# Kernel tuning notes

Measured on AMD Instinct MI355X. Metric: run time of the kernel, lower is better.

The kernel has to match this reference:

```python
import jax, jax.numpy as jnp
import numpy as np


def _softmax_kernel(data, proj, is_query, eps=1e-4):
    # data: [b,h,n,d], proj: [m,d] -> features [b,h,n,m]
    d = data.shape[-1]
    data_normalizer = d ** -0.25
    ratio = proj.shape[0] ** -0.5
    data_dash = jnp.einsum('bhnd,md->bhnm', data_normalizer * data, proj)
    diag_data = jnp.sum(data * data, axis=-1, keepdims=True) * 0.5 * (data_normalizer ** 2)
    if is_query:
        stab = jnp.max(data_dash, axis=-1, keepdims=True)
    else:
        stab = jnp.max(data_dash, axis=(-1, -2), keepdims=True)
    stab = jax.lax.stop_gradient(stab)
    return ratio * (jnp.exp(data_dash - diag_data - stab) + eps)


def setup_inputs() -> dict:
    key = jax.random.key(0)
    k1, k2, k3, k4 = jax.random.split(key, 4)
    b, h, n, d, m = 8, 16, 4096, 64, 256
    q = jax.random.normal(k1, (b, h, n, d), dtype=jnp.float32)
    k = jax.random.normal(k2, (b, h, n, d), dtype=jnp.float32)
    v = jax.random.normal(k3, (b, h, n, d), dtype=jnp.float32)
    projection_matrix = jax.random.normal(k4, (m, d), dtype=jnp.float32)
    return {'q': q, 'k': k, 'v': v, 'projection_matrix': projection_matrix}


def reference(q, k, v, projection_matrix):
    # FAVOR+ softmax-kernel features
    q_prime = _softmax_kernel(q, projection_matrix, is_query=True)   # [b,h,n,m]
    k_prime = _softmax_kernel(k, projection_matrix, is_query=False)  # [b,h,n,m]
    # Non-causal linear attention
    k_sum = jnp.sum(k_prime, axis=-2)                                # [b,h,m]
    d_inv = 1.0 / jnp.einsum('bhnm,bhm->bhn', q_prime, k_sum)        # [b,h,n]
    context = jnp.einsum('bhnm,bhne->bhme', k_prime, v)              # [b,h,m,e]
    out = jnp.einsum('bhme,bhnm,bhn->bhne', context, q_prime, d_inv) # [b,h,n,e]
    return out
```

## Files before the change

### kernel.cpp

```cpp
#include <hip/hip_runtime.h>


#define BH 128
#define NN 4096
#define DD 64
#define MM 256
#define NORM 0.35355339059327373f
#define EPS 1e-4f

typedef unsigned short u16;
typedef __attribute__((ext_vector_type(8))) short bfrag;
typedef __attribute__((ext_vector_type(4))) float ffrag;
#define MFMA16(A,B,C) __builtin_amdgcn_mfma_f32_16x16x32_bf16(A,B,C,0,0,0)

__device__ __forceinline__ float u2f(u16 h){ return __uint_as_float(((unsigned)h)<<16); }
__device__ __forceinline__ void splitf(float x, u16 &h, u16 &l){
    unsigned uh = __float_as_uint(x) & 0xffff0000u;
    h = (u16)(uh >> 16);
    float r = x - __uint_as_float(uh);
    l = (u16)(__float_as_uint(r) >> 16);
}

__global__ void p0_proj(const float* __restrict__ proj, u16* __restrict__ phi, u16* __restrict__ plo){
    int idx = blockIdx.x*256 + threadIdx.x;
    u16 h,l; splitf(proj[idx], h, l);
    phi[idx] = h; plo[idx] = l;
}

__global__ __launch_bounds__(256) void p0_vt(const float* __restrict__ vin,
        u16* __restrict__ vthi, u16* __restrict__ vtlo, float* __restrict__ vsum){
    int head = blockIdx.x >> 6;
    int n0 = (blockIdx.x & 63) * 64;
    int t = threadIdx.x;
    __shared__ float tile[64][65];
    {
        int row = t >> 2, c0 = (t & 3) * 16;
        const float* src = vin + ((size_t)head*NN + n0 + row)*64 + c0;
        #pragma unroll
        for (int i=0;i<4;++i){
            float4 x = *(const float4*)(src + i*4);
            tile[row][c0+i*4+0]=x.x; tile[row][c0+i*4+1]=x.y;
            tile[row][c0+i*4+2]=x.z; tile[row][c0+i*4+3]=x.w;
        }
    }
    __syncthreads();
    {
        int e = t >> 2, nq = (t & 3) * 16;
        float s = 0.f;
        unsigned ph[8], pl[8];
        #pragma unroll
        for (int jj=0;jj<8;++jj){
            float x0 = tile[nq+jj*2+0][e];
            float x1 = tile[nq+jj*2+1][e];
            s += x0 + x1;
            u16 h0,l0,h1,l1; splitf(x0,h0,l0); splitf(x1,h1,l1);
            ph[jj] = (unsigned)h0 | ((unsigned)h1<<16);
            pl[jj] = (unsigned)l0 | ((unsigned)l1<<16);
        }
        size_t base = ((size_t)head*64 + e)*NN + n0 + nq;
        uint4 a0; a0.x=ph[0]; a0.y=ph[1]; a0.z=ph[2]; a0.w=ph[3];
        uint4 a1; a1.x=ph[4]; a1.y=ph[5]; a1.z=ph[6]; a1.w=ph[7];
        uint4 b0; b0.x=pl[0]; b0.y=pl[1]; b0.z=pl[2]; b0.w=pl[3];
        uint4 b1; b1.x=pl[4]; b1.y=pl[5]; b1.z=pl[6]; b1.w=pl[7];
        *(uint4*)(vthi + base)     = a0;
        *(uint4*)(vthi + base + 8) = a1;
        *(uint4*)(vtlo + base)     = b0;
        *(uint4*)(vtlo + base + 8) = b1;
        s += __shfl_xor(s, 1);
        s += __shfl_xor(s, 2);
        if ((t & 3) == 0) atomicAdd(vsum + head*64 + e, s);
    }
}

__global__ __launch_bounds__(256) __attribute__((amdgpu_waves_per_eu(2,2)))
void kc_kernel(
        const float* __restrict__ kin, const u16* __restrict__ phi, const u16* __restrict__ plo,
        const u16* __restrict__ vthi, const u16* __restrict__ vtlo,
        float* __restrict__ ctxPart, float* __restrict__ mbArr)
{
    const int blk  = blockIdx.x;
    const int head = blk >> 3;
    const int n0   = (blk & 7) * 512;
    const int t    = threadIdx.x;
    const int w    = t >> 6;
    const int lane = t & 63;
    const int qd   = lane >> 4;
    const int li   = lane & 15;

    __shared__ __attribute__((aligned(16))) u16 knh[32*64], knl[32*64];
    __shared__ __attribute__((aligned(16))) u16 bsh[256*32], bsl[256*32];
    __shared__ float diag_s[32];
    __shared__ float wmax[4];

    bfrag pf[4][2][2];
    #pragma unroll
    for (int mt=0;mt<4;++mt){
        int m = w*64 + mt*16 + li;
        #pragma unroll
        for (int ks=0;ks<2;++ks){
            pf[mt][ks][0] = *(const bfrag*)(phi + m*64 + ks*32 + qd*8);
            pf[mt][ks][1] = *(const bfrag*)(plo + m*64 + ks*32 + qd*8);
        }
    }

    ffrag acc[4][4];
    #pragma unroll
    for (int et=0;et<4;++et)
        #pragma unroll
        for (int mt=0;mt<4;++mt){ ffrag z = {0.f,0.f,0.f,0.f}; acc[et][mt] = z; }
    float ks[4] = {0.f,0.f,0.f,0.f};
    float M = -3.0e38f;

    const float* kg = kin + ((size_t)head*NN + n0)*64;

    for (int sub=0; sub<16; ++sub){
        {
            int row = t >> 3;
            int g   = t & 7;
            const float* src = kg + (size_t)(sub*32 + row)*64 + g*8;
            float4 x0 = *(const float4*)(src);
            float4 x1 = *(const float4*)(src + 4);
            float xs[8] = {x0.x,x0.y,x0.z,x0.w,x1.x,x1.y,x1.z,x1.w};
            bfrag hv, lv;
            float ss = 0.f;
            #pragma unroll
            for (int j=0;j<8;++j){
                float xn = xs[j]*NORM;
                ss += xn*xn;
                u16 hh,ll; splitf(xn,hh,ll);
                hv[j] = (short)hh; lv[j] = (short)ll;
            }
            int gs = g ^ (row & 7);
            *(bfrag*)(knh + row*64 + gs*8) = hv;
            *(bfrag*)(knl + row*64 + gs*8) = lv;
            ss += __shfl_xor(ss, 1);
            ss += __shfl_xor(ss, 2);
            ss += __shfl_xor(ss, 4);
            if ((t & 7) == 0) diag_s[row] = 0.5f*ss;
        }
        __syncthreads();

        ffrag d1[2][4];
        #pragma unroll
        for (int nt=0;nt<2;++nt)
            #pragma unroll
            for (int mt=0;mt<4;++mt){ ffrag z = {0.f,0.f,0.f,0.f}; d1[nt][mt] = z; }
        #pragma unroll
        for (int nt=0;nt<2;++nt){
            int n = nt*16 + li;
            bfrag ah[2], al[2];
            #pragma unroll
            for (int kss=0;kss<2;++kss){
                int gp = (kss*4 + qd) ^ (n & 7);
                ah[kss] = *(const bfrag*)(knh + n*64 + gp*8);
                al[kss] = *(const bfrag*)(knl + n*64 + gp*8);
            }
            #pragma unroll
            for (int mt=0;mt<4;++mt){
                #pragma unroll
                for (int kss=0;kss<2;++kss){
                    d1[nt][mt] = MFMA16(ah[kss], pf[mt][kss][0], d1[nt][mt]);
                    d1[nt][mt] = MFMA16(ah[kss], pf[mt][kss][1], d1[nt][mt]);
                    d1[nt][mt] = MFMA16(al[kss], pf[mt][kss][0], d1[nt][mt]);
                }
            }
        }

        float mx = -3.0e38f;
        #pragma unroll
        for (int nt=0;nt<2;++nt)
            #pragma unroll
            for (int mt=0;mt<4;++mt)
                #pragma unroll
                for (int rg=0;rg<4;++rg) mx = fmaxf(mx, d1[nt][mt][rg]);
        mx = fmaxf(mx, __shfl_xor(mx, 1));
        mx = fmaxf(mx, __shfl_xor(mx, 2));
        mx = fmaxf(mx, __shfl_xor(mx, 4));
        mx = fmaxf(mx, __shfl_xor(mx, 8));
        mx = fmaxf(mx, __shfl_xor(mx, 16));
        mx = fmaxf(mx, __shfl_xor(mx, 32));
        if (lane == 0) wmax[w] = mx;
        __syncthreads();
        float Ms = fmaxf(fmaxf(wmax[0],wmax[1]), fmaxf(wmax[2],wmax[3]));
        float Mn = fmaxf(M, Ms);
        float r  = __expf(M - Mn);
        M = Mn;
        #pragma unroll
        for (int mt=0;mt<4;++mt) ks[mt] *= r;
        #pragma unroll
        for (int et=0;et<4;++et)
            #pragma unroll
            for (int mt=0;mt<4;++mt)
                #pragma unroll
                for (int rg=0;rg<4;++rg) acc[et][mt][rg] *= r;

        float sl[4] = {0.f,0.f,0.f,0.f};
        #pragma unroll
        for (int nt=0;nt<2;++nt){
            float d4[4];
            #pragma unroll
            for (int rg=0;rg<4;++rg) d4[rg] = diag_s[nt*16 + qd*4 + rg];
            #pragma unroll
            for (int mt=0;mt<4;++mt){
                int m = w*64 + mt*16 + li;
                u16 h4[4], l4[4];
                #pragma unroll
                for (int rg=0;rg<4;++rg){
                    float f = __expf(d1[nt][mt][rg] - d4[rg] - M);
                    sl[mt] += f;
                    splitf(f, h4[rg], l4[rg]);
                }
                int g  = nt*2 + (qd>>1);
                int gp = g ^ ((m>>1)&3);
                int off = m*32 + gp*8 + (qd&1)*4;
                *(ushort4*)(bsh + off) = make_ushort4(h4[0],h4[1],h4[2],h4[3]);
                *(ushort4*)(bsl + off) = make_ushort4(l4[0],l4[1],l4[2],l4[3]);
            }
        }
        #pragma unroll
        for (int mt=0;mt<4;++mt){
            float v = sl[mt];
            v += __shfl_xor(v, 16);
            v += __shfl_xor(v, 32);
            ks[mt] += v;
        }
        __syncthreads();

        bfrag bh[4], bl[4];
        #pragma unroll
        for (int mt=0;mt<4;++mt){
            int m = w*64 + mt*16 + li;
            int gp = qd ^ ((m>>1)&3);
            bh[mt] = *(const bfrag*)(bsh + m*32 + gp*8);
            bl[mt] = *(const bfrag*)(bsl + m*32 + gp*8);
        }
        #pragma unroll
        for (int et=0;et<4;++et){
            int e = et*16 + li;
            size_t vb = ((size_t)head*64 + e)*NN + n0 + sub*32 + qd*8;
            bfrag avh = *(const bfrag*)(vthi + vb);
            bfrag avl = *(const bfrag*)(vtlo + vb);
            #pragma unroll
            for (int mt=0;mt<4;++mt){
                acc[et][mt] = MFMA16(avh, bh[mt], acc[et][mt]);
                acc[et][mt] = MFMA16(avh, bl[mt], acc[et][mt]);
                acc[et][mt] = MFMA16(avl, bh[mt], acc[et][mt]);
            }
        }
        __syncthreads();
    }

    float* P = ctxPart + (size_t)blk * (65*256);
    #pragma unroll
    for (int et=0;et<4;++et)
        #pragma unroll
        for (int mt=0;mt<4;++mt)
            #pragma unroll
            for (int rg=0;rg<4;++rg){
                int e = et*16 + qd*4 + rg;
                int m = w*64 + mt*16 + li;
                P[e*256 + m] = acc[et][mt][rg];
            }
    if (qd == 0){
        #pragma unroll
        for (int mt=0;mt<4;++mt) P[64*256 + w*64 + mt*16 + li] = ks[mt];
    }
    if (t == 0) mbArr[blk] = M;
}

__global__ __launch_bounds__(256) void kred(const float* __restrict__ ctxPart,
        const float* __restrict__ mbArr, const float* __restrict__ vsum,
        u16* __restrict__ ctxh, u16* __restrict__ ctxl, float* __restrict__ ksumG){
    int head = blockIdx.x / 65;
    int e = blockIdx.x % 65;
    int m = threadIdx.x;
    float mb[8];
    float mk = -3.0e38f;
    #pragma unroll
    for (int c=0;c<8;++c){ mb[c] = mbArr[head*8+c]; mk = fmaxf(mk, mb[c]); }
    float s = 0.f;
    #pragma unroll
    for (int c=0;c<8;++c){
        float sc = __expf(mb[c] - mk);
        s += sc * ctxPart[((size_t)(head*8+c)*65 + e)*256 + m];
    }
    if (e == 64){
        ksumG[head*256 + m] = s + 4096.0f*EPS;
    } else {
        float val = s + EPS * vsum[head*64 + e];
        u16 h,l; splitf(val,h,l);
        ctxh[((size_t)head*64 + e)*256 + m] = h;
        ctxl[((size_t)head*64 + e)*256 + m] = l;
    }
}

__global__ __launch_bounds__(256) __attribute__((amdgpu_waves_per_eu(2,2)))
void k3_kernel(
        const float* __restrict__ qin, const u16* __restrict__ phi, const u16* __restrict__ plo,
        const u16* __restrict__ ctxh, const u16* __restrict__ ctxl,
        const float* __restrict__ ksumG, float* __restrict__ out)
{
    const int bx   = blockIdx.x;
    const int head = (bx & 7) + 8 * ((bx >> 3) & 15);
    const int n0   = (bx >> 7) * 64;
    const int t    = threadIdx.x;
    const int w    = t >> 6;
    const int lane = t & 63;
    const int qd   = lane >> 4;
    const int li   = lane & 15;

    __shared__ __attribute__((aligned(16))) u16 SM[32768];
    u16* qnh = SM;
    u16* qnl = SM + 4096;
    u16* fh  = SM;
    u16* fl  = SM + 16384;
    __shared__ float diagq[64], drm[64], dinvs[64], wm[4][64];

    {
        int row = t >> 2;
        const float* src = qin + ((size_t)head*NN + n0 + row)*64 + (t&3)*16;
        float ss = 0.f;
        #pragma unroll
        for (int gi=0; gi<2; ++gi){
            int g = (t&3)*2 + gi;
            float4 x0 = *(const float4*)(src + gi*8);
            float4 x1 = *(const float4*)(src + gi*8 + 4);
            float xs[8] = {x0.x,x0.y,x0.z,x0.w,x1.x,x1.y,x1.z,x1.w};
            bfrag hv, lv;
            #pragma unroll
            for (int j=0;j<8;++j){
                float xn = xs[j]*NORM;
                ss += xn*xn;
                u16 hh,ll; splitf(xn,hh,ll);
                hv[j] = (short)hh; lv[j] = (short)ll;
            }
            int gs = g ^ (row & 7);
            *(bfrag*)(qnh + row*64 + gs*8) = hv;
            *(bfrag*)(qnl + row*64 + gs*8) = lv;
        }
        ss += __shfl_xor(ss, 1);
        ss += __shfl_xor(ss, 2);
        if ((t&3) == 0) diagq[row] = 0.5f*ss;
    }

    float4 ks4[4];
    #pragma unroll
    for (int mt=0;mt<4;++mt)
        ks4[mt] = *(const float4*)(ksumG + head*256 + w*64 + mt*16 + qd*4);
    __syncthreads();

    ffrag d1[4][4];
    #pragma unroll
    for (int mt=0;mt<4;++mt)
        #pragma unroll
        for (int nt=0;nt<4;++nt){ ffrag z = {0.f,0.f,0.f,0.f}; d1[mt][nt] = z; }
    #pragma unroll
    for (int kss=0;kss<2;++kss){
        bfrag pfh[4], pfl[4];
        #pragma unroll
        for (int mt=0;mt<4;++mt){
            int m = w*64 + mt*16 + li;
            pfh[mt] = *(const bfrag*)(phi + m*64 + kss*32 + qd*8);
            pfl[mt] = *(const bfrag*)(plo + m*64 + kss*32 + qd*8);
        }
        #pragma unroll
        for (int nt=0;nt<4;++nt){
            int n = nt*16 + li;
            int gp = (kss*4 + qd) ^ (n & 7);
            bfrag bh = *(const bfrag*)(qnh + n*64 + gp*8);
            bfrag bl = *(const bfrag*)(qnl + n*64 + gp*8);
            #pragma unroll
            for (int mt=0;mt<4;++mt){
                d1[mt][nt] = MFMA16(pfh[mt], bh, d1[mt][nt]);
                d1[mt][nt] = MFMA16(pfh[mt], bl, d1[mt][nt]);
                d1[mt][nt] = MFMA16(pfl[mt], bh, d1[mt][nt]);
            }
        }
    }

    #pragma unroll
    for (int nt=0;nt<4;++nt){
        float mx = -3.0e38f;
        #pragma unroll
        for (int mt=0;mt<4;++mt)
            #pragma unroll
            for (int rg=0;rg<4;++rg) mx = fmaxf(mx, d1[mt][nt][rg]);
        mx = fmaxf(mx, __shfl_xor(mx, 16));
        mx = fmaxf(mx, __shfl_xor(mx, 32));
        if (qd == 0) wm[w][nt*16 + li] = mx;
    }
    __syncthreads();
    if (t < 64)
        drm[t] = diagq[t] + fmaxf(fmaxf(wm[0][t], wm[1][t]), fmaxf(wm[2][t], wm[3][t]));
    __syncthreads();

    float ds[4] = {0.f,0.f,0.f,0.f};
    #pragma unroll
    for (int nt=0;nt<4;++nt){
        int n = nt*16 + li;
        float dr = drm[n];
        #pragma unroll
        for (int mt=0;mt<4;++mt){
            float fv[4];
            u16 h4[4], l4[4];
            #pragma unroll
            for (int rg=0;rg<4;++rg){
                fv[rg] = __expf(d1[mt][nt][rg] - dr) + EPS;
                splitf(fv[rg], h4[rg], l4[rg]);
            }
            ds[nt] += fv[0]*ks4[mt].x + fv[1]*ks4[mt].y + fv[2]*ks4[mt].z + fv[3]*ks4[mt].w;
            int G  = w*8 + mt*2 + (qd>>1);
            int Gp = G ^ (li & 7);
            int off = n*256 + Gp*8 + (qd&1)*4;
            *(ushort4*)(fh + off) = make_ushort4(h4[0],h4[1],h4[2],h4[3]);
            *(ushort4*)(fl + off) = make_ushort4(l4[0],l4[1],l4[2],l4[3]);
        }
    }
    #pragma unroll
    for (int nt=0;nt<4;++nt){
        float v = ds[nt];
        v += __shfl_xor(v, 16);
        v += __shfl_xor(v, 32);
        if (qd == 0) wm[w][nt*16 + li] = v;
    }
    __syncthreads();
    if (t < 64)
        dinvs[t] = 1.0f / (wm[0][t] + wm[1][t] + wm[2][t] + wm[3][t]);
    __syncthreads();

    ffrag a2[4];
    #pragma unroll
    for (int nt=0;nt<4;++nt){ ffrag z = {0.f,0.f,0.f,0.f}; a2[nt] = z; }
    const u16* cbh = ctxh + (size_t)head*64*256 + (w*16 + li)*256;
    const u16* cbl = ctxl + (size_t)head*64*256 + (w*16 + li)*256;
    #pragma unroll
    for (int ksm=0; ksm<8; ++ksm){
        bfrag ch = *(const bfrag*)(cbh + ksm*32 + qd*8);
        bfrag cl = *(const bfrag*)(cbl + ksm*32 + qd*8);
        #pragma unroll
        for (int nt=0;nt<4;++nt){
            int n = nt*16 + li;
            int Gp = (ksm*4 + qd) ^ (li & 7);
            bfrag ah2 = *(const bfrag*)(fh + n*256 + Gp*8);
            bfrag al2 = *(const bfrag*)(fl + n*256 + Gp*8);
            a2[nt] = MFMA16(ah2, ch, a2[nt]);
            a2[nt] = MFMA16(ah2, cl, a2[nt]);
            a2[nt] = MFMA16(al2, ch, a2[nt]);
        }
    }

    float* og = out + ((size_t)head*NN + n0)*64;
    #pragma unroll
    for (int nt=0;nt<4;++nt){
        #pragma unroll
        for (int rg=0;rg<4;++rg){
            int n = nt*16 + qd*4 + rg;
            og[(size_t)n*64 + w*16 + li] = a2[nt][rg] * dinvs[n];
        }
    }
}

extern "C" void kernel_launch(void* const* d_in, const int* in_sizes, int n_in,
                              void* d_out, int out_size, void* d_ws, size_t ws_size,
                              hipStream_t stream) {
    const float* q    = (const float*)d_in[0];
    const float* k    = (const float*)d_in[1];
    const float* v    = (const float*)d_in[2];
    const float* proj = (const float*)d_in[3];
    float* out = (float*)d_out;

    char* wp = (char*)d_ws;
    u16* phi     = (u16*)wp;  wp += (size_t)MM*DD*2;
    u16* plo     = (u16*)wp;  wp += (size_t)MM*DD*2;
    u16* vthi    = (u16*)wp;  wp += (size_t)BH*64*NN*2;
    u16* vtlo    = (u16*)wp;  wp += (size_t)BH*64*NN*2;
    float* vsum  = (float*)wp; wp += (size_t)BH*64*4;
    float* mbArr = (float*)wp; wp += (size_t)1024*4;
    float* ctxPart = (float*)wp; wp += (size_t)1024*65*256*4;
    u16* ctxh    = (u16*)wp;  wp += (size_t)BH*64*256*2;
    u16* ctxl    = (u16*)wp;  wp += (size_t)BH*64*256*2;
    float* ksumG = (float*)wp; wp += (size_t)BH*256*4;

    hipMemsetAsync(vsum, 0, (size_t)BH*64*4, stream);
    p0_proj<<<64, 256, 0, stream>>>(proj, phi, plo);
    p0_vt<<<BH*64, 256, 0, stream>>>(v, vthi, vtlo, vsum);
    kc_kernel<<<1024, 256, 0, stream>>>(k, phi, plo, vthi, vtlo, ctxPart, mbArr);
    kred<<<BH*65, 256, 0, stream>>>(ctxPart, mbArr, vsum, ctxh, ctxl, ksumG);
    k3_kernel<<<BH*64, 256, 0, stream>>>(q, phi, plo, ctxh, ctxl, ksumG, out);
}
```

Baseline: 707.8 us.

## Process q features in two half chunks to halve k3 LDS and raise occupancy

The k3 kernel now builds and consumes the q-feature tile in two 32-row chunks instead of one 64-row tile. This halves the shared-memory buffer from 64KB to 32KB, and the occupancy hint goes from 2 to 4 waves per EU so more blocks can be resident to hide latency. The cost is extra barriers per chunk, the context fragments being reloaded from global memory once per chunk, and tighter register limits that could cause spills given the large d1 accumulator array.

```diff
diff --git a/kernel.cpp b/kernel.cpp
--- a/kernel.cpp
+++ b/kernel.cpp
@@ -294,7 +294,7 @@
     }
 }
 
-__global__ __launch_bounds__(256) __attribute__((amdgpu_waves_per_eu(2,2)))
+__global__ __launch_bounds__(256) __attribute__((amdgpu_waves_per_eu(4,4)))
 void k3_kernel(
         const float* __restrict__ qin, const u16* __restrict__ phi, const u16* __restrict__ plo,
         const u16* __restrict__ ctxh, const u16* __restrict__ ctxl,
@@ -309,11 +309,11 @@
     const int qd   = lane >> 4;
     const int li   = lane & 15;
 
-    __shared__ __attribute__((aligned(16))) u16 SM[32768];
+    __shared__ __attribute__((aligned(16))) u16 SM[16384];
     u16* qnh = SM;
     u16* qnl = SM + 4096;
     u16* fh  = SM;
-    u16* fl  = SM + 16384;
+    u16* fl  = SM + 8192;
     __shared__ float diagq[64], drm[64], dinvs[64], wm[4][64];
 
     {
@@ -394,59 +394,63 @@
         drm[t] = diagq[t] + fmaxf(fmaxf(wm[0][t], wm[1][t]), fmaxf(wm[2][t], wm[3][t]));
     __syncthreads();
 
-    float ds[4] = {0.f,0.f,0.f,0.f};
-    #pragma unroll
-    for (int nt=0;nt<4;++nt){
-        int n = nt*16 + li;
-        float dr = drm[n];
-        #pragma unroll
-        for (int mt=0;mt<4;++mt){
-            float fv[4];
-            u16 h4[4], l4[4];
-            #pragma unroll
-            for (int rg=0;rg<4;++rg){
-                fv[rg] = __expf(d1[mt][nt][rg] - dr) + EPS;
-                splitf(fv[rg], h4[rg], l4[rg]);
-            }
-            ds[nt] += fv[0]*ks4[mt].x + fv[1]*ks4[mt].y + fv[2]*ks4[mt].z + fv[3]*ks4[mt].w;
-            int G  = w*8 + mt*2 + (qd>>1);
-            int Gp = G ^ (li & 7);
-            int off = n*256 + Gp*8 + (qd&1)*4;
-            *(ushort4*)(fh + off) = make_ushort4(h4[0],h4[1],h4[2],h4[3]);
-            *(ushort4*)(fl + off) = make_ushort4(l4[0],l4[1],l4[2],l4[3]);
-        }
-    }
-    #pragma unroll
-    for (int nt=0;nt<4;++nt){
-        float v = ds[nt];
-        v += __shfl_xor(v, 16);
-        v += __shfl_xor(v, 32);
-        if (qd == 0) wm[w][nt*16 + li] = v;
-    }
-    __syncthreads();
-    if (t < 64)
-        dinvs[t] = 1.0f / (wm[0][t] + wm[1][t] + wm[2][t] + wm[3][t]);
-    __syncthreads();
-
     ffrag a2[4];
     #pragma unroll
     for (int nt=0;nt<4;++nt){ ffrag z = {0.f,0.f,0.f,0.f}; a2[nt] = z; }
     const u16* cbh = ctxh + (size_t)head*64*256 + (w*16 + li)*256;
     const u16* cbl = ctxl + (size_t)head*64*256 + (w*16 + li)*256;
-    #pragma unroll
-    for (int ksm=0; ksm<8; ++ksm){
-        bfrag ch = *(const bfrag*)(cbh + ksm*32 + qd*8);
-        bfrag cl = *(const bfrag*)(cbl + ksm*32 + qd*8);
-        #pragma unroll
-        for (int nt=0;nt<4;++nt){
+
+    #pragma unroll
+    for (int ch=0; ch<2; ++ch){
+        #pragma unroll
+        for (int ntl=0; ntl<2; ++ntl){
+            const int nt = ch*2 + ntl;
             int n = nt*16 + li;
-            int Gp = (ksm*4 + qd) ^ (li & 7);
-            bfrag ah2 = *(const bfrag*)(fh + n*256 + Gp*8);
-            bfrag al2 = *(const bfrag*)(fl + n*256 + Gp*8);
-            a2[nt] = MFMA16(ah2, ch, a2[nt]);
-            a2[nt] = MFMA16(ah2, cl, a2[nt]);
-            a2[nt] = MFMA16(al2, ch, a2[nt]);
-        }
+            float dr = drm[n];
+            float ds = 0.f;
+            #pragma unroll
+            for (int mt=0;mt<4;++mt){
+                float fv[4];
+                u16 h4[4], l4[4];
+                #pragma unroll
+                for (int rg=0;rg<4;++rg){
+                    fv[rg] = __expf(d1[mt][nt][rg] - dr) + EPS;
+                    splitf(fv[rg], h4[rg], l4[rg]);
+                }
+                ds += fv[0]*ks4[mt].x + fv[1]*ks4[mt].y + fv[2]*ks4[mt].z + fv[3]*ks4[mt].w;
+                int G  = w*8 + mt*2 + (qd>>1);
+                int Gp = G ^ (li & 7);
+                int off = (ntl*16 + li)*256 + Gp*8 + (qd&1)*4;
+                *(ushort4*)(fh + off) = make_ushort4(h4[0],h4[1],h4[2],h4[3]);
+                *(ushort4*)(fl + off) = make_ushort4(l4[0],l4[1],l4[2],l4[3]);
+            }
+            ds += __shfl_xor(ds, 16);
+            ds += __shfl_xor(ds, 32);
+            if (qd == 0) wm[w][n] = ds;
+        }
+        __syncthreads();
+
+        if (t < 32){
+            int n = ch*32 + t;
+            dinvs[n] = 1.0f / (wm[0][n] + wm[1][n] + wm[2][n] + wm[3][n]);
+        }
+
+        #pragma unroll
+        for (int ksm=0; ksm<8; ++ksm){
+            bfrag chv = *(const bfrag*)(cbh + ksm*32 + qd*8);
+            bfrag clv = *(const bfrag*)(cbl + ksm*32 + qd*8);
+            #pragma unroll
+            for (int ntl=0; ntl<2; ++ntl){
+                int nl = ntl*16 + li;
+                int Gp = (ksm*4 + qd) ^ (li & 7);
+                bfrag ah2 = *(const bfrag*)(fh + nl*256 + Gp*8);
+                bfrag al2 = *(const bfrag*)(fl + nl*256 + Gp*8);
+                a2[ch*2+ntl] = MFMA16(ah2, chv, a2[ch*2+ntl]);
+                a2[ch*2+ntl] = MFMA16(ah2, clv, a2[ch*2+ntl]);
+                a2[ch*2+ntl] = MFMA16(al2, chv, a2[ch*2+ntl]);
+            }
+        }
+        __syncthreads();
     }
 
     float* og = out + ((size_t)head*NN + n0)*64;
```

Measured after the change: 732.6 us. 3.5% more time.
